# Kernel optimization log

Measured on AMD Instinct MI355X. Metric: run time of the kernel, lower is better.

The kernel has to match this reference:

```python
import jax, jax.numpy as jnp
import numpy as np
from jax import lax
import math

S, V, D, L, B = 64, 50257, 586, 4, 32  # seq_len, num_tokens, num_inputs, num_layers, batch_size
K1 = S // 4 + 1   # 17, conv1 kernel
P1 = S // 16 + 1  # 5,  avgpool1 kernel
P2 = S // 32 + 1  # 3,  avgpool2 kernel
EPS = 1e-5


def setup_inputs() -> dict:
    key = jax.random.key(0)
    ks = jax.random.split(key, 14)
    tokens = jax.random.randint(ks[0], (S, B), 0, V)
    emb = jax.random.normal(ks[1], (V, D - 3), jnp.float32) * 0.02
    # pos_embeds = randn(S,1,3).repeat(1,B,1)
    pos = jnp.tile(jax.random.normal(ks[2], (S, 1, 3), jnp.float32), (1, B, 1))
    gamma = 1.0 + 0.1 * jax.random.normal(ks[3], (L, S), jnp.float32)
    beta = 0.1 * jax.random.normal(ks[4], (L, S), jnp.float32)
    w1 = jax.random.normal(ks[5], (B // 2, B, K1), jnp.float32) * 0.02
    b1 = jax.random.normal(ks[6], (B // 2,), jnp.float32) * 0.02
    w2 = jax.random.normal(ks[7], (B // 4, B // 2, 1), jnp.float32) * 0.02
    b2 = jax.random.normal(ks[8], (B // 4,), jnp.float32) * 0.02
    w3 = jax.random.normal(ks[9], (B, B // 4, 3), jnp.float32) * 0.02
    b3 = jax.random.normal(ks[10], (B,), jnp.float32) * 0.02
    wl = jax.random.normal(ks[11], (128, 36), jnp.float32) * 0.1
    bl = jax.random.normal(ks[12], (128,), jnp.float32) * 0.1
    return {"tokens": tokens, "emb": emb, "pos": pos, "gamma": gamma, "beta": beta,
            "w1": w1, "b1": b1, "w2": w2, "b2": b2, "w3": w3, "b3": b3,
            "wl": wl, "bl": bl}


def _conv1d(x, w, b):
    # x: (N, C_in, Lx), w: (C_out, C_in, K)
    y = lax.conv_general_dilated(x, w, (1,), 'VALID',
                                 dimension_numbers=('NCH', 'OIH', 'NCH'))
    return y + b[None, :, None]


def _avgpool1d(x, k):
    # torch AvgPool1d: stride=kernel, floor mode
    n, c, lx = x.shape
    lo = lx // k
    return x[:, :, :lo * k].reshape(n, c, lo, k).mean(axis=-1)


def _logits(tokens, emb, pos, gamma, beta, w1, b1, w2, b2, w3, b3, wl, bl):
    x = emb[tokens] * math.sqrt(D)          # (S, B, D-3)
    x = jnp.concatenate([x, pos], axis=2)   # (S, B, D)
    for l in range(L):
        xb = x.swapaxes(0, 1)               # (B, S, D): BatchNorm1d over channels=S
        mean = xb.mean(axis=(0, 2), keepdims=True)
        var = xb.var(axis=(0, 2), keepdims=True)  # biased, training-mode batch stats
        xb = gamma[l][None, :, None] * (xb - mean) * lax.rsqrt(var + EPS) + beta[l][None, :, None]
        x = xb.swapaxes(0, 1)
    out = _conv1d(x, w1, b1)                # (S, B/2, D-16) = (64, 16, 570)
    out = _avgpool1d(out, P1)               # (64, 16, 114)
    out = _conv1d(out, w2, b2)              # (64, 8, 114)
    out = _avgpool1d(out, P2)               # (64, 8, 38)
    out = _conv1d(out, w3, b3)              # (64, 32, 36)
    out = jnp.einsum('sbk,vk->sbv', out, wl) + bl  # (64, 32, 128)
    return out


def reference(tokens, emb, pos, gamma, beta, w1, b1, w2, b2, w3, b3, wl, bl):
    out = _logits(tokens, emb, pos, gamma, beta, w1, b1, w2, b2, w3, b3, wl, bl)
    # vectorized replacement for the triple-nested .item() argmax loop
    return jnp.argmax(out, axis=-1).astype(jnp.float32)  # (S, B)
```

## Files before the change

### kernel.cpp

```cpp
#include <hip/hip_runtime.h>
#include <math.h>

#define SS 64
#define BB 32
#define DD 586
#define DE 583
#define U1 114
#define U2 38
#define T3 36
#define NTOK 18752
#define NSTAT (SS*BB)
#define SQD 24.207436873820409f


__global__ __launch_bounds__(256) void k_main(
    const int* __restrict__ tokens, const float* __restrict__ emb,
    const float* __restrict__ pos, const float* __restrict__ w1,
    double* __restrict__ rowsumd, double* __restrict__ rowsqd,
    float* __restrict__ part)
{
  const int s = blockIdx.x, g = blockIdx.y;
  const int tid = threadIdx.x;
  __shared__ float xs[8*DD];
  __shared__ int stok[8];
  if (tid < 8) stok[tid] = tokens[s*BB + g*8 + tid];
  __syncthreads();
  {
    const int rr = tid >> 5, l = tid & 31;
    const float* row = emb + (size_t)stok[rr]*DE;
    double sum = 0.0, sq = 0.0;
    #pragma unroll
    for (int j = 0; j < 19; ++j) {
      int d = l + 32*j;
      if (d < DD) {
        float v = (d < DE) ? row[d] * SQD
                           : pos[(s*BB + g*8 + rr)*3 + (d - DE)];
        xs[rr*DD + d] = v;
        sum += v; sq += (double)v*v;
      }
    }
    for (int off = 16; off > 0; off >>= 1) {
      sum += __shfl_down(sum, off, 32);
      sq  += __shfl_down(sq, off, 32);
    }
    if (l == 0) {
      rowsumd[s*BB + g*8 + rr] = sum;
      rowsqd [s*BB + g*8 + rr] = sq;
    }
  }
  __syncthreads();
  const int up = tid & 127;
  const int oh = __builtin_amdgcn_readfirstlane(tid >> 7);
  const int u  = (up < U1) ? up : (U1 - 1);
  float acc[8] = {0,0,0,0,0,0,0,0};
  for (int cc = 0; cc < 8; ++cc) {
    const float* xr = &xs[cc*DD + 5*u];
    float xv[21];
    #pragma unroll
    for (int m = 0; m < 21; ++m) xv[m] = xr[m];
    float xw[17];
    #pragma unroll
    for (int k = 0; k < 17; ++k)
      xw[k] = ((xv[k] + xv[k+1]) + (xv[k+2] + xv[k+3])) + xv[k+4];
    #pragma unroll
    for (int j = 0; j < 8; ++j) {
      const float* wj = w1 + ((size_t)(oh*8 + j)*BB + (g*8 + cc))*17;
      float a = 0.f;
      #pragma unroll
      for (int k = 0; k < 17; ++k) a += xw[k] * wj[k];
      acc[j] += a;
    }
  }
  if (up < U1) {
    float* pb = part + ((size_t)(g*SS + s)*16 + oh*8)*U1 + up;
    #pragma unroll
    for (int j = 0; j < 8; ++j) pb[j*U1] = acc[j] * 0.2f;
  }
}

__global__ __launch_bounds__(256) void k_tail(
    const double* __restrict__ rowsumd, const double* __restrict__ rowsqd,
    const float* __restrict__ gamma, const float* __restrict__ beta,
    const float* __restrict__ part, const float* __restrict__ w1,
    const float* __restrict__ b1, const float* __restrict__ w2,
    const float* __restrict__ b2, const float* __restrict__ w3,
    const float* __restrict__ b3, const float* __restrict__ wl,
    const float* __restrict__ bl, float* __restrict__ out)
{
  const int s = blockIdx.x, tid = threadIdx.x;
  __shared__ float o2[16*U1];
  __shared__ float p2[16*U2];
  __shared__ float o4[8*U2];
  __shared__ float o5[32*T3];
  __shared__ float wlb[128*37];
  __shared__ float blb[128];
  __shared__ float wsumb[16];
  __shared__ float sAl, sDe;
  for (int idx = tid; idx < 128*36; idx += 256) {
    int v = idx / 36, t = idx - v*36;
    wlb[v*37 + t] = wl[idx];
  }
  if (tid < 128) blb[tid] = bl[tid];
  {
    const int o = tid >> 4, i = tid & 15;
    float acc = 0.f;
    for (int j = i; j < BB*17; j += 16) acc += w1[o*BB*17 + j];
    for (int off = 8; off > 0; off >>= 1) acc += __shfl_down(acc, off, 16);
    if (i == 0) wsumb[o] = acc;
  }
  if (tid < 32) {
    double sm = rowsumd[s*BB + tid], qq = rowsqd[s*BB + tid];
    for (int off = 16; off > 0; off >>= 1) {
      sm += __shfl_down(sm, off, 32);
      qq += __shfl_down(qq, off, 32);
    }
    if (tid == 0) {
      double m0d = sm / (double)NTOK;
      float m0 = (float)m0d;
      float v0 = (float)(qq / (double)NTOK - m0d*m0d);
      float a = 1.0f;
      for (int l = 0; l < 4; ++l) {
        float r = 1.0f / sqrtf(a*a*v0 + 1e-5f);
        a = gamma[l*SS + s] * r * a;
      }
      sAl = a;
      sDe = beta[3*SS + s] - a*m0;
    }
  }
  __syncthreads();
  const float al = sAl, de = sDe;
  for (int idx = tid; idx < 16*U1; idx += 256) {
    int o = idx / U1;
    float psum = part[(size_t)(0*SS + s)*16*U1 + idx]
               + part[(size_t)(1*SS + s)*16*U1 + idx]
               + part[(size_t)(2*SS + s)*16*U1 + idx]
               + part[(size_t)(3*SS + s)*16*U1 + idx];
    o2[idx] = al*psum + de*wsumb[o] + b1[o];
  }
  __syncthreads();
  for (int i2 = tid; i2 < 16*U2; i2 += 256) {
    int o = i2 / U2, v = i2 - o*U2;
    p2[i2] = (o2[o*U1 + 3*v] + o2[o*U1 + 3*v+1] + o2[o*U1 + 3*v+2]) * (1.f/3.f);
  }
  __syncthreads();
  for (int i2 = tid; i2 < 8*U2; i2 += 256) {
    int p = i2 / U2, v = i2 - p*U2;
    float acc = b2[p];
    #pragma unroll
    for (int o = 0; o < 16; ++o) acc += p2[o*U2 + v] * w2[p*16 + o];
    o4[i2] = acc;
  }
  __syncthreads();
  for (int i2 = tid; i2 < 32*T3; i2 += 256) {
    int q = i2 / T3, t = i2 - q*T3;
    float acc = b3[q];
    #pragma unroll
    for (int p = 0; p < 8; ++p) {
      acc += o4[p*U2 + t    ] * w3[(q*8+p)*3 + 0]
           + o4[p*U2 + t + 1] * w3[(q*8+p)*3 + 1]
           + o4[p*U2 + t + 2] * w3[(q*8+p)*3 + 2];
    }
    o5[i2] = acc;
  }
  __syncthreads();
  const int q = tid >> 3, vs = tid & 7;
  float best = -1e30f; int bidx = 0;
  const float* orow = &o5[q*T3];
  for (int i = 0; i < 16; ++i) {
    int v = vs + 8*i;
    float acc = blb[v];
    const float* wr = &wlb[v*37];
    #pragma unroll
    for (int t = 0; t < 36; ++t) acc += orow[t] * wr[t];
    if (acc > best) { best = acc; bidx = v; }
  }
  #pragma unroll
  for (int off = 1; off < 8; off <<= 1) {
    float ov = __shfl_xor(best, off);
    int oi = __shfl_xor(bidx, off);
    if (ov > best || (ov == best && oi < bidx)) { best = ov; bidx = oi; }
  }
  if (vs == 0) out[s*BB + q] = (float)bidx;
}

extern "C" void kernel_launch(void* const* d_in, const int* in_sizes, int n_in,
                              void* d_out, int out_size, void* d_ws, size_t ws_size,
                              hipStream_t stream)
{
  const int*   tokens = (const int*)  d_in[0];
  const float* emb    = (const float*)d_in[1];
  const float* pos    = (const float*)d_in[2];
  const float* gamma  = (const float*)d_in[3];
  const float* beta   = (const float*)d_in[4];
  const float* w1     = (const float*)d_in[5];
  const float* b1     = (const float*)d_in[6];
  const float* w2     = (const float*)d_in[7];
  const float* b2     = (const float*)d_in[8];
  const float* w3     = (const float*)d_in[9];
  const float* b3     = (const float*)d_in[10];
  const float* wl     = (const float*)d_in[11];
  const float* bl     = (const float*)d_in[12];
  float* out = (float*)d_out;

  double* rowsumd = (double*)d_ws;
  double* rowsqd  = rowsumd + NSTAT;
  float*  part    = (float*)(rowsqd + NSTAT);

  k_main<<<dim3(SS, 4), dim3(256), 0, stream>>>(
      tokens, emb, pos, w1, rowsumd, rowsqd, part);
  k_tail<<<dim3(SS), dim3(256), 0, stream>>>(
      rowsumd, rowsqd, gamma, beta, part, w1, b1, w2, b2, w3, b3,
      wl, bl, out);
}
```

Measured before the change: 193.5 us.

## Fuse main and tail kernels using last-block-done atomic counter per sequence row

```diff
diff --git a/kernel.cpp b/kernel.cpp
--- a/kernel.cpp
+++ b/kernel.cpp
@@ -13,18 +13,47 @@
 #define SQD 24.207436873820409f
 
 
-__global__ __launch_bounds__(256) void k_main(
+__global__ __launch_bounds__(256) void k_fused(
     const int* __restrict__ tokens, const float* __restrict__ emb,
-    const float* __restrict__ pos, const float* __restrict__ w1,
+    const float* __restrict__ pos, const float* __restrict__ gamma,
+    const float* __restrict__ beta, const float* __restrict__ w1,
+    const float* __restrict__ b1, const float* __restrict__ w2,
+    const float* __restrict__ b2, const float* __restrict__ w3,
+    const float* __restrict__ b3, const float* __restrict__ wl,
+    const float* __restrict__ bl,
     double* __restrict__ rowsumd, double* __restrict__ rowsqd,
-    float* __restrict__ part)
+    float* __restrict__ part, int* __restrict__ counter,
+    float* __restrict__ out)
 {
   const int s = blockIdx.x, g = blockIdx.y;
   const int tid = threadIdx.x;
   __shared__ float xs[8*DD];
+  __shared__ float wlb[128*37];
+  __shared__ float blb[128];
+  __shared__ float wsumb[16];
   __shared__ int stok[8];
+  __shared__ int isLast;
+  __shared__ float sAl, sDe;
+  __shared__ float o2[16*U1];
+  __shared__ float p2[16*U2];
+  __shared__ float o4[8*U2];
+  __shared__ float o5[32*T3];
+
   if (tid < 8) stok[tid] = tokens[s*BB + g*8 + tid];
-  __syncthreads();
+  for (int idx = tid; idx < 128*36; idx += 256) {
+    int v = idx / 36, t = idx - v*36;
+    wlb[v*37 + t] = wl[idx];
+  }
+  if (tid < 128) blb[tid] = bl[tid];
+  {
+    const int o = tid >> 4, i = tid & 15;
+    float acc = 0.f;
+    for (int j = i; j < BB*17; j += 16) acc += w1[o*BB*17 + j];
+    for (int off = 8; off > 0; off >>= 1) acc += __shfl_down(acc, off, 16);
+    if (i == 0) wsumb[o] = acc;
+  }
+  __syncthreads();
+
   {
     const int rr = tid >> 5, l = tid & 31;
     const float* row = emb + (size_t)stok[rr]*DE;
@@ -49,6 +78,7 @@
     }
   }
   __syncthreads();
+
   const int up = tid & 127;
   const int oh = __builtin_amdgcn_readfirstlane(tid >> 7);
   const int u  = (up < U1) ? up : (U1 - 1);
@@ -76,38 +106,18 @@
     #pragma unroll
     for (int j = 0; j < 8; ++j) pb[j*U1] = acc[j] * 0.2f;
   }
-}
-
-__global__ __launch_bounds__(256) void k_tail(
-    const double* __restrict__ rowsumd, const double* __restrict__ rowsqd,
-    const float* __restrict__ gamma, const float* __restrict__ beta,
-    const float* __restrict__ part, const float* __restrict__ w1,
-    const float* __restrict__ b1, const float* __restrict__ w2,
-    const float* __restrict__ b2, const float* __restrict__ w3,
-    const float* __restrict__ b3, const float* __restrict__ wl,
-    const float* __restrict__ bl, float* __restrict__ out)
-{
-  const int s = blockIdx.x, tid = threadIdx.x;
-  __shared__ float o2[16*U1];
-  __shared__ float p2[16*U2];
-  __shared__ float o4[8*U2];
-  __shared__ float o5[32*T3];
-  __shared__ float wlb[128*37];
-  __shared__ float blb[128];
-  __shared__ float wsumb[16];
-  __shared__ float sAl, sDe;
-  for (int idx = tid; idx < 128*36; idx += 256) {
-    int v = idx / 36, t = idx - v*36;
-    wlb[v*37 + t] = wl[idx];
-  }
-  if (tid < 128) blb[tid] = bl[tid];
-  {
-    const int o = tid >> 4, i = tid & 15;
-    float acc = 0.f;
-    for (int j = i; j < BB*17; j += 16) acc += w1[o*BB*17 + j];
-    for (int off = 8; off > 0; off >>= 1) acc += __shfl_down(acc, off, 16);
-    if (i == 0) wsumb[o] = acc;
-  }
+
+  __threadfence();
+  __syncthreads();
+  if (tid == 0) {
+    int old = __hip_atomic_fetch_add(&counter[s], 1, __ATOMIC_ACQ_REL,
+                                     __HIP_MEMORY_SCOPE_AGENT);
+    isLast = (old == 3);
+  }
+  __syncthreads();
+  if (!isLast) return;
+  __threadfence();
+
   if (tid < 32) {
     double sm = rowsumd[s*BB + tid], qq = rowsqd[s*BB + tid];
     for (int off = 16; off > 0; off >>= 1) {
@@ -145,22 +155,22 @@
   __syncthreads();
   for (int i2 = tid; i2 < 8*U2; i2 += 256) {
     int p = i2 / U2, v = i2 - p*U2;
-    float acc = b2[p];
-    #pragma unroll
-    for (int o = 0; o < 16; ++o) acc += p2[o*U2 + v] * w2[p*16 + o];
-    o4[i2] = acc;
+    float a2 = b2[p];
+    #pragma unroll
+    for (int o = 0; o < 16; ++o) a2 += p2[o*U2 + v] * w2[p*16 + o];
+    o4[i2] = a2;
   }
   __syncthreads();
   for (int i2 = tid; i2 < 32*T3; i2 += 256) {
     int q = i2 / T3, t = i2 - q*T3;
-    float acc = b3[q];
+    float a3 = b3[q];
     #pragma unroll
     for (int p = 0; p < 8; ++p) {
-      acc += o4[p*U2 + t    ] * w3[(q*8+p)*3 + 0]
-           + o4[p*U2 + t + 1] * w3[(q*8+p)*3 + 1]
-           + o4[p*U2 + t + 2] * w3[(q*8+p)*3 + 2];
-    }
-    o5[i2] = acc;
+      a3 += o4[p*U2 + t    ] * w3[(q*8+p)*3 + 0]
+          + o4[p*U2 + t + 1] * w3[(q*8+p)*3 + 1]
+          + o4[p*U2 + t + 2] * w3[(q*8+p)*3 + 2];
+    }
+    o5[i2] = a3;
   }
   __syncthreads();
   const int q = tid >> 3, vs = tid & 7;
@@ -168,11 +178,11 @@
   const float* orow = &o5[q*T3];
   for (int i = 0; i < 16; ++i) {
     int v = vs + 8*i;
-    float acc = blb[v];
+    float a4 = blb[v];
     const float* wr = &wlb[v*37];
     #pragma unroll
-    for (int t = 0; t < 36; ++t) acc += orow[t] * wr[t];
-    if (acc > best) { best = acc; bidx = v; }
+    for (int t = 0; t < 36; ++t) a4 += orow[t] * wr[t];
+    if (a4 > best) { best = a4; bidx = v; }
   }
   #pragma unroll
   for (int off = 1; off < 8; off <<= 1) {
@@ -205,10 +215,10 @@
   double* rowsumd = (double*)d_ws;
   double* rowsqd  = rowsumd + NSTAT;
   float*  part    = (float*)(rowsqd + NSTAT);
-
-  k_main<<<dim3(SS, 4), dim3(256), 0, stream>>>(
-      tokens, emb, pos, w1, rowsumd, rowsqd, part);
-  k_tail<<<dim3(SS), dim3(256), 0, stream>>>(
-      rowsumd, rowsqd, gamma, beta, part, w1, b1, w2, b2, w3, b3,
-      wl, bl, out);
+  int*    counter = (int*)(part + 4*SS*16*U1);
+
+  (void)hipMemsetAsync(counter, 0, SS*sizeof(int), stream);
+  k_fused<<<dim3(SS, 4), dim3(256), 0, stream>>>(
+      tokens, emb, pos, gamma, beta, w1, b1, w2, b2, w3, b3, wl, bl,
+      rowsumd, rowsqd, part, counter, out);
 }
```

After: 227.4 us. +17.5%, slower.
